# Kernel tuning notes

Hardware: AMD Instinct MI355X
Metric: run time of the kernel (lower is better)

Reference implementation:

```python
import jax, jax.numpy as jnp
import numpy as np

HIDDEN = 768
INTER = 3072
HEADS = 12
HEAD_DIM = INTER // HEADS  # 256
LN_EPS = 1e-6
R_SOFTPLUS_0 = 1.442695041


def setup_inputs() -> dict:
    key = jax.random.key(0)
    ks = jax.random.split(key, 12)
    s = 0.02
    inp = {
        "hidden_states": jax.random.normal(ks[0], (8, 4096, HIDDEN), dtype=jnp.float32),
        "pooling_query": jax.random.normal(ks[1], (1, 1, HIDDEN), dtype=jnp.float32) * s,
        "Wq": jax.random.normal(ks[2], (HIDDEN, INTER), dtype=jnp.float32) * s,
        "bq": jnp.zeros((INTER,), dtype=jnp.float32),
        "Wk": jax.random.normal(ks[3], (HIDDEN, INTER), dtype=jnp.float32) * s,
        "bk": jnp.zeros((INTER,), dtype=jnp.float32),
        "Wv": jax.random.normal(ks[4], (HIDDEN, INTER), dtype=jnp.float32) * s,
        "bv": jnp.zeros((INTER,), dtype=jnp.float32),
        "Wp": jax.random.normal(ks[5], (INTER, HIDDEN), dtype=jnp.float32) * s,
        "bp": jnp.zeros((HIDDEN,), dtype=jnp.float32),
        "per_dim_scale": jnp.zeros((HEAD_DIM,), dtype=jnp.float32),
        "ln_w": jnp.ones((HIDDEN,), dtype=jnp.float32),
        "ln_b": jnp.zeros((HIDDEN,), dtype=jnp.float32),
    }
    return inp


def reference(hidden_states, pooling_query, Wq, bq, Wk, bk, Wv, bv, Wp, bp,
              per_dim_scale, ln_w, ln_b):
    B, S, _ = hidden_states.shape
    dt = hidden_states.dtype

    # Query: single pooling token, identical across batch -> [H, D]
    q = (pooling_query.reshape(1, HIDDEN) @ Wq + bq).reshape(HEADS, HEAD_DIM)
    # PerDimScale: q * (r_softplus0/sqrt(D)) * softplus(per_dim_scale)
    scale = (R_SOFTPLUS_0 / np.sqrt(HEAD_DIM)).astype(np.float32)
    q = q * (scale * jax.nn.softplus(per_dim_scale))

    # K/V projections: [B, S, H, D]
    k = (hidden_states @ Wk + bk).reshape(B, S, HEADS, HEAD_DIM)
    v = (hidden_states @ Wv + bv).reshape(B, S, HEADS, HEAD_DIM)

    # Single-query attention: logits [B, H, S]; scaling=1.0 (scale_logits_by_head_dims=False)
    # logit cap skipped (no_attention_logit_cap=True)
    logits = jnp.einsum("hd,bshd->bhs", q, k)
    attn = jax.nn.softmax(logits.astype(jnp.float32), axis=-1).astype(dt)

    # Weighted sum over seq: [B, H, D] -> concat heads -> [B, H*D]
    ctx = jnp.einsum("bhs,bshd->bhd", attn, v).reshape(B, HEADS * HEAD_DIM)

    out = ctx @ Wp + bp  # [B, HIDDEN]
    # LayerNorm; note the original forward adds ones to ln weight in-place each call,
    # so effective weight for one call is (ln_w + 1).
    mean = jnp.mean(out, axis=-1, keepdims=True)
    var = jnp.var(out, axis=-1, keepdims=True)
    out = (out - mean) * jax.lax.rsqrt(var + LN_EPS) * (ln_w + 1.0) + ln_b

    pooled = out[:, None, :]  # [B, 1, HIDDEN]
    attn_weights = attn[:, :, None, :]  # [B, H, 1, S]
    return pooled, attn_weights
```

## Files before the change

### kernel.cpp

```cpp
#include <hip/hip_runtime.h>
#include <cstdint>
#include <cmath>

#define LN_EPS 1e-6f

#define N_QCH 24u
#define O_QPART 0u
#define O_Q     73728u
#define O_WK    76800u
#define O_PLOG  86016u
#define O_PHP   1658880u
#define N_SC    32
#define O_CTXP  4091904u
#define N_CCH   12
#define O_OUTP  4411392u
#define N_ICH   48

__device__ __forceinline__ float waveReduceSum(float v) {
#pragma unroll
    for (int o = 32; o >= 1; o >>= 1) v += __shfl_xor(v, o, 64);
    return v;
}
__device__ __forceinline__ float waveReduceMax(float v) {
#pragma unroll
    for (int o = 32; o >= 1; o >>= 1) v = fmaxf(v, __shfl_xor(v, o, 64));
    return v;
}

__global__ __launch_bounds__(256) void k1_qpart(const float* __restrict__ pq,
                                                const float* __restrict__ Wq,
                                                float* __restrict__ ws) {
    int h = blockIdx.x % 12;
    int ch = blockIdx.x / 12;
    int tid = threadIdx.x;
    int col = h * 256 + tid;
    int c0 = ch * 32;
    float acc = 0.f;
#pragma unroll 8
    for (int i = 0; i < 32; ++i) {
        int c = c0 + i;
        acc += pq[c] * Wq[c * 3072 + col];
    }
    ws[O_QPART + ch * 3072 + col] = acc;
}

__global__ __launch_bounds__(256) void k1b_qreduce(const float* __restrict__ bq,
                                                   const float* __restrict__ pds,
                                                   float* __restrict__ ws) {
    int j = blockIdx.x * 256 + threadIdx.x;
    float acc = bq[j];
#pragma unroll
    for (unsigned ch = 0; ch < N_QCH; ++ch) acc += ws[O_QPART + ch * 3072 + j];
    float x = pds[j & 255];
    float sp = (x > 20.f) ? x : log1pf(expf(x));
    const float scale = 1.442695041f / 16.0f;
    ws[O_Q + j] = acc * scale * sp;
}

__global__ __launch_bounds__(256) void k2_wkeff(const float* __restrict__ Wk,
                                                float* __restrict__ ws) {
    int c = blockIdx.x;
    int tid = threadIdx.x;
    int w = tid >> 6, lane = tid & 63;
    const float4* wk = reinterpret_cast<const float4*>(Wk + (size_t)c * 3072);
    const float4* qv = reinterpret_cast<const float4*>(ws + O_Q);
#pragma unroll
    for (int i = 0; i < 3; ++i) {
        int h = w * 3 + i;
        float4 a = wk[h * 64 + lane];
        float4 b = qv[h * 64 + lane];
        float d = a.x * b.x + a.y * b.y + a.z * b.z + a.w * b.w;
        d = waveReduceSum(d);
        if (lane == 0) ws[O_WK + c * 12 + h] = d;
    }
}

__global__ __launch_bounds__(256) void k3_logits(const float* __restrict__ hidden,
                                                 float* __restrict__ ws) {
    __shared__ float4 tile4[1536];
    __shared__ float4 wkb4[576];
    int blk = blockIdx.x;
    int q = blk & 3;
    int st = (blk >> 2) & 63;
    int b = blk >> 8;
    int s0 = st * 64;
    const float* hb = hidden + (size_t)(b * 4096 + s0) * 768;
    const float4* wkg4 = reinterpret_cast<const float4*>(ws + O_WK);
    int tid = threadIdx.x;
    int w = tid >> 6, lane = tid & 63;
    int rr[6], jj6[6];
#pragma unroll
    for (int it = 0; it < 6; ++it) {
        int idx = it * 256 + tid;
        rr[it] = idx / 24;
        jj6[it] = idx % 24;
    }
    for (int i = tid; i < 576; i += 256) wkb4[i] = wkg4[q * 576 + i];
    float4 v[6];
#pragma unroll
    for (int it = 0; it < 6; ++it)
        v[it] = reinterpret_cast<const float4*>(hb + rr[it] * 768 + q * 192)[jj6[it]];

    float acc[12];
#pragma unroll
    for (int h = 0; h < 12; ++h) acc[h] = 0.f;

#pragma unroll
    for (int cph = 0; cph < 2; ++cph) {
#pragma unroll
        for (int it = 0; it < 6; ++it)
            tile4[rr[it] * 24 + (jj6[it] ^ (rr[it] & 7))] = v[it];
        if (cph == 0) {
#pragma unroll
            for (int it = 0; it < 6; ++it)
                v[it] = reinterpret_cast<const float4*>(hb + rr[it] * 768 + q * 192 + 96)[jj6[it]];
        }
        __syncthreads();
#pragma unroll
        for (int jj = 0; jj < 6; ++jj) {
            int jcol = w * 6 + jj;
            float4 x = tile4[lane * 24 + (jcol ^ (lane & 7))];
            const float4* wr = &wkb4[cph * 288 + jcol * 12];
            float xc[4] = {x.x, x.y, x.z, x.w};
#pragma unroll
            for (int cc = 0; cc < 4; ++cc) {
                float4 w0 = wr[cc * 3 + 0], w1 = wr[cc * 3 + 1], w2 = wr[cc * 3 + 2];
                acc[0] += xc[cc] * w0.x;  acc[1] += xc[cc] * w0.y;  acc[2]  += xc[cc] * w0.z;  acc[3]  += xc[cc] * w0.w;
                acc[4] += xc[cc] * w1.x;  acc[5] += xc[cc] * w1.y;  acc[6]  += xc[cc] * w1.z;  acc[7]  += xc[cc] * w1.w;
                acc[8] += xc[cc] * w2.x;  acc[9] += xc[cc] * w2.y;  acc[10] += xc[cc] * w2.z;  acc[11] += xc[cc] * w2.w;
            }
        }
        __syncthreads();
    }
    float* red = reinterpret_cast<float*>(tile4);
#pragma unroll
    for (int h = 0; h < 12; ++h) red[(w * 12 + h) * 64 + lane] = acc[h];
    __syncthreads();
    float* plog = ws + O_PLOG;
    for (int idx = tid; idx < 768; idx += 256) {
        int h = idx / 64, r2 = idx & 63;
        float v2 = red[(0 + h) * 64 + r2] + red[(12 + h) * 64 + r2] +
                   red[(24 + h) * 64 + r2] + red[(36 + h) * 64 + r2];
        plog[(size_t)q * 393216 + (size_t)(b * 12 + h) * 4096 + s0 + r2] = v2;
    }
}

__global__ __launch_bounds__(256) void k4_softmax(const float* __restrict__ ws,
                                                  float* __restrict__ attn) {
    __shared__ float sh[4];
    int row = blockIdx.x;
    const float4* p0 = reinterpret_cast<const float4*>(ws + O_PLOG + (size_t)row * 4096);
    const float4* p1 = p0 + 98304;
    const float4* p2 = p0 + 196608;
    const float4* p3 = p0 + 294912;
    float* base = attn + (size_t)row * 4096;
    int tid = threadIdx.x;
    float4 x[4];
#pragma unroll
    for (int t = 0; t < 4; ++t) {
        float4 a = p0[t * 256 + tid], c = p1[t * 256 + tid];
        float4 d = p2[t * 256 + tid], e = p3[t * 256 + tid];
        x[t].x = (a.x + c.x) + (d.x + e.x);
        x[t].y = (a.y + c.y) + (d.y + e.y);
        x[t].z = (a.z + c.z) + (d.z + e.z);
        x[t].w = (a.w + c.w) + (d.w + e.w);
    }
    float m = -1e30f;
#pragma unroll
    for (int t = 0; t < 4; ++t)
        m = fmaxf(m, fmaxf(fmaxf(x[t].x, x[t].y), fmaxf(x[t].z, x[t].w)));
    m = waveReduceMax(m);
    if ((tid & 63) == 0) sh[tid >> 6] = m;
    __syncthreads();
    m = fmaxf(fmaxf(sh[0], sh[1]), fmaxf(sh[2], sh[3]));
    __syncthreads();
    float s = 0.f;
#pragma unroll
    for (int t = 0; t < 4; ++t) {
        x[t].x = expf(x[t].x - m); x[t].y = expf(x[t].y - m);
        x[t].z = expf(x[t].z - m); x[t].w = expf(x[t].w - m);
        s += x[t].x + x[t].y + x[t].z + x[t].w;
    }
    s = waveReduceSum(s);
    if ((tid & 63) == 0) sh[tid >> 6] = s;
    __syncthreads();
    s = sh[0] + sh[1] + sh[2] + sh[3];
    float inv = 1.0f / s;
#pragma unroll
    for (int t = 0; t < 4; ++t) {
        x[t].x *= inv; x[t].y *= inv; x[t].z *= inv; x[t].w *= inv;
        reinterpret_cast<float4*>(base)[t * 256 + tid] = x[t];
    }
}

__global__ __launch_bounds__(256) void k5_phpart(const float* __restrict__ hidden,
                                                 const float* __restrict__ attn,
                                                 float* __restrict__ ws) {
    __shared__ float4 sh4[12 * 4 * 64];
    int blk = blockIdx.x;
    int sc = blk & 31;
    int ct = (blk >> 5) % 3;
    int b = blk / 96;
    int tid = threadIdx.x;
    int w = tid >> 6, lane = tid & 63;
    int c = ct * 256 + lane * 4;
    int s0 = sc * 128;
    const float* hb = hidden + (size_t)(b * 4096 + s0) * 768 + c;
    const float* ab = attn + (size_t)b * 49152 + s0 + w;
    float4 acc[12];
#pragma unroll
    for (int h = 0; h < 12; ++h) acc[h] = make_float4(0.f, 0.f, 0.f, 0.f);
    for (int g = 0; g < 32; ++g) {
        float4 x = *reinterpret_cast<const float4*>(hb + (size_t)(g * 4 + w) * 768);
        float a[12];
#pragma unroll
        for (int h = 0; h < 12; ++h) a[h] = ab[h * 4096 + g * 4];
#pragma unroll
        for (int h = 0; h < 12; ++h) {
            acc[h].x += a[h] * x.x; acc[h].y += a[h] * x.y;
            acc[h].z += a[h] * x.z; acc[h].w += a[h] * x.w;
        }
    }
#pragma unroll
    for (int h = 0; h < 12; ++h) sh4[(h * 4 + w) * 64 + lane] = acc[h];
    __syncthreads();
    float* php = ws + O_PHP;
#pragma unroll
    for (int i = 0; i < 3; ++i) {
        int h = w * 3 + i;
        float4 a = sh4[(h * 4 + 0) * 64 + lane];
        float4 b2 = sh4[(h * 4 + 1) * 64 + lane];
        float4 c2 = sh4[(h * 4 + 2) * 64 + lane];
        float4 d = sh4[(h * 4 + 3) * 64 + lane];
        float4 r;
        r.x = (a.x + b2.x) + (c2.x + d.x);
        r.y = (a.y + b2.y) + (c2.y + d.y);
        r.z = (a.z + b2.z) + (c2.z + d.z);
        r.w = (a.w + b2.w) + (c2.w + d.w);
        *reinterpret_cast<float4*>(php + (size_t)(sc * 96 + b * 12 + h) * 768 + c) = r;
    }
}

__global__ __launch_bounds__(256) void k7_ctxpart(const float* __restrict__ Wv,
                                                  float* __restrict__ ws) {
    __shared__ float phl[512];
    int blk = blockIdx.x;
    int jt = blk % 12, cch = blk / 12;
    int tid = threadIdx.x;
    const float* php = ws + O_PHP;
#pragma unroll
    for (int t = 0; t < 2; ++t) {
        int idx = t * 256 + tid;
        int b = idx >> 6, cc = idx & 63;
        int c = cch * 64 + cc;
        const float* p = php + (size_t)(b * 12 + jt) * 768 + c;
        float s = 0.f;
#pragma unroll
        for (int sc = 0; sc < N_SC; ++sc) s += p[(size_t)sc * 73728];
        phl[idx] = s;
    }
    __syncthreads();
    int j = jt * 256 + tid;
    float acc[8];
#pragma unroll
    for (int b = 0; b < 8; ++b) acc[b] = 0.f;
    for (int cc = 0; cc < 64; ++cc) {
        int c = cch * 64 + cc;
        float wv = Wv[(size_t)c * 3072 + j];
#pragma unroll
        for (int b = 0; b < 8; ++b) acc[b] += phl[b * 64 + cc] * wv;
    }
#pragma unroll
    for (int b = 0; b < 8; ++b)
        ws[O_CTXP + (size_t)(cch * 8 + b) * 3072 + j] = acc[b];
}

__global__ __launch_bounds__(256) void k8_outpart(const float* __restrict__ Wp,
                                                  const float* __restrict__ bv,
                                                  float* __restrict__ ws) {
    __shared__ float ctxl[512];
    int blk = blockIdx.x;
    int jt = blk % 3, ich = blk / 3;
    int tid = threadIdx.x;
#pragma unroll
    for (int t = 0; t < 2; ++t) {
        int idx = t * 256 + tid;
        int b = idx >> 6, ii = idx & 63;
        int i = ich * 64 + ii;
        float s = bv[i];
#pragma unroll
        for (int cch = 0; cch < N_CCH; ++cch)
            s += ws[O_CTXP + (size_t)(cch * 8 + b) * 3072 + i];
        ctxl[idx] = s;
    }
    __syncthreads();
    int j = jt * 256 + tid;
    float acc[8];
#pragma unroll
    for (int b = 0; b < 8; ++b) acc[b] = 0.f;
    for (int ii = 0; ii < 64; ++ii) {
        int i = ich * 64 + ii;
        float wp = Wp[(size_t)i * 768 + j];
#pragma unroll
        for (int b = 0; b < 8; ++b) acc[b] += ctxl[b * 64 + ii] * wp;
    }
#pragma unroll
    for (int b = 0; b < 8; ++b)
        ws[O_OUTP + (size_t)(ich * 8 + b) * 768 + j] = acc[b];
}

__global__ __launch_bounds__(256) void k9_ln(const float* __restrict__ bp,
                                             const float* __restrict__ ln_w,
                                             const float* __restrict__ ln_b,
                                             const float* __restrict__ ws,
                                             float* __restrict__ pooled) {
    __shared__ float sh[8];
    int b = blockIdx.x, tid = threadIdx.x;
    const float* op = ws + O_OUTP;
    float vals[3];
    float lsum = 0.f, lsq = 0.f;
#pragma unroll
    for (int t = 0; t < 3; ++t) {
        int j = t * 256 + tid;
        float v = bp[j];
#pragma unroll
        for (int ich = 0; ich < N_ICH; ++ich) v += op[(size_t)(ich * 8 + b) * 768 + j];
        vals[t] = v; lsum += v; lsq += v * v;
    }
    lsum = waveReduceSum(lsum);
    lsq = waveReduceSum(lsq);
    if ((tid & 63) == 0) { sh[tid >> 6] = lsum; sh[4 + (tid >> 6)] = lsq; }
    __syncthreads();
    float mean = (sh[0] + sh[1] + sh[2] + sh[3]) * (1.f / 768.f);
    float var = (sh[4] + sh[5] + sh[6] + sh[7]) * (1.f / 768.f) - mean * mean;
    float inv = rsqrtf(var + LN_EPS);
#pragma unroll
    for (int t = 0; t < 3; ++t) {
        int j = t * 256 + tid;
        pooled[b * 768 + j] = (vals[t] - mean) * inv * (ln_w[j] + 1.f) + ln_b[j];
    }
}

extern "C" void kernel_launch(void* const* d_in, const int* in_sizes, int n_in,
                              void* d_out, int out_size, void* d_ws, size_t ws_size,
                              hipStream_t stream) {
    const float* hidden = (const float*)d_in[0];
    const float* pq     = (const float*)d_in[1];
    const float* Wq     = (const float*)d_in[2];
    const float* bq     = (const float*)d_in[3];
    const float* Wk     = (const float*)d_in[4];
    const float* Wv     = (const float*)d_in[6];
    const float* bv     = (const float*)d_in[7];
    const float* Wp     = (const float*)d_in[8];
    const float* bp     = (const float*)d_in[9];
    const float* pds    = (const float*)d_in[10];
    const float* ln_w   = (const float*)d_in[11];
    const float* ln_b   = (const float*)d_in[12];
    float* out = (float*)d_out;
    float* ws  = (float*)d_ws;
    float* pooled = out;
    float* attn   = out + 6144;

    k1_qpart   <<<288, 256, 0, stream>>>(pq, Wq, ws);
    k1b_qreduce<<<12, 256, 0, stream>>>(bq, pds, ws);
    k2_wkeff   <<<768, 256, 0, stream>>>(Wk, ws);
    k3_logits  <<<2048, 256, 0, stream>>>(hidden, ws);
    k4_softmax <<<96, 256, 0, stream>>>(ws, attn);
    k5_phpart  <<<768, 256, 0, stream>>>(hidden, attn, ws);
    k7_ctxpart <<<144, 256, 0, stream>>>(Wv, ws);
    k8_outpart <<<144, 256, 0, stream>>>(Wp, bv, ws);
    k9_ln      <<<8, 256, 0, stream>>>(bp, ln_w, ln_b, ws, pooled);
}
```

Before: 271.8 us.

## Double-buffer k3_logits LDS tile in four smaller chunks, drop trailing barrier

The logits kernel now stages each 64-row slice of hidden states in four 48-column chunks instead of two 96-column chunks. It ping-pongs between two shared-memory buffers, so the barrier at the end of each chunk iteration can be removed. Each thread holds three prefetched float4 registers instead of six, which lowers register pressure and may allow higher occupancy. The cost is more loop iterations with less work per barrier and a narrower XOR swizzle that could raise LDS bank conflicts.

After: 266.7 us (median of 2 runs). Within noise of the previous version (-1.9%).

```diff
diff --git a/kernel.cpp b/kernel.cpp
--- a/kernel.cpp
+++ b/kernel.cpp
@@ -77,50 +77,50 @@
 
 __global__ __launch_bounds__(256) void k3_logits(const float* __restrict__ hidden,
                                                  float* __restrict__ ws) {
-    __shared__ float4 tile4[1536];
+    __shared__ float4 tile4[2][768];
     __shared__ float4 wkb4[576];
     int blk = blockIdx.x;
     int q = blk & 3;
     int st = (blk >> 2) & 63;
     int b = blk >> 8;
     int s0 = st * 64;
-    const float* hb = hidden + (size_t)(b * 4096 + s0) * 768;
+    const float* hb = hidden + (size_t)(b * 4096 + s0) * 768 + q * 192;
     const float4* wkg4 = reinterpret_cast<const float4*>(ws + O_WK);
     int tid = threadIdx.x;
     int w = tid >> 6, lane = tid & 63;
-    int rr[6], jj6[6];
-#pragma unroll
-    for (int it = 0; it < 6; ++it) {
-        int idx = it * 256 + tid;
-        rr[it] = idx / 24;
-        jj6[it] = idx % 24;
-    }
     for (int i = tid; i < 576; i += 256) wkb4[i] = wkg4[q * 576 + i];
-    float4 v[6];
-#pragma unroll
-    for (int it = 0; it < 6; ++it)
-        v[it] = reinterpret_cast<const float4*>(hb + rr[it] * 768 + q * 192)[jj6[it]];
+    int rr[3], jj[3];
+#pragma unroll
+    for (int t = 0; t < 3; ++t) {
+        int idx = t * 256 + tid;
+        rr[t] = idx / 12;
+        jj[t] = idx % 12;
+    }
+    float4 v[3];
+#pragma unroll
+    for (int t = 0; t < 3; ++t)
+        v[t] = *reinterpret_cast<const float4*>(hb + rr[t] * 768 + jj[t] * 4);
 
     float acc[12];
 #pragma unroll
     for (int h = 0; h < 12; ++h) acc[h] = 0.f;
 
-#pragma unroll
-    for (int cph = 0; cph < 2; ++cph) {
-#pragma unroll
-        for (int it = 0; it < 6; ++it)
-            tile4[rr[it] * 24 + (jj6[it] ^ (rr[it] & 7))] = v[it];
-        if (cph == 0) {
-#pragma unroll
-            for (int it = 0; it < 6; ++it)
-                v[it] = reinterpret_cast<const float4*>(hb + rr[it] * 768 + q * 192 + 96)[jj6[it]];
+    for (int ck = 0; ck < 4; ++ck) {
+        float4* buf = tile4[ck & 1];
+#pragma unroll
+        for (int t = 0; t < 3; ++t)
+            buf[rr[t] * 12 + (jj[t] ^ (rr[t] & 3))] = v[t];
+        if (ck < 3) {
+#pragma unroll
+            for (int t = 0; t < 3; ++t)
+                v[t] = *reinterpret_cast<const float4*>(hb + rr[t] * 768 + (ck + 1) * 48 + jj[t] * 4);
         }
         __syncthreads();
 #pragma unroll
-        for (int jj = 0; jj < 6; ++jj) {
-            int jcol = w * 6 + jj;
-            float4 x = tile4[lane * 24 + (jcol ^ (lane & 7))];
-            const float4* wr = &wkb4[cph * 288 + jcol * 12];
+        for (int j2 = 0; j2 < 3; ++j2) {
+            int jcol = w * 3 + j2;
+            float4 x = buf[lane * 12 + (jcol ^ (lane & 3))];
+            const float4* wr = &wkb4[(ck * 48 + jcol * 4) * 3];
             float xc[4] = {x.x, x.y, x.z, x.w};
 #pragma unroll
             for (int cc = 0; cc < 4; ++cc) {
@@ -130,7 +130,6 @@
                 acc[8] += xc[cc] * w2.x;  acc[9] += xc[cc] * w2.y;  acc[10] += xc[cc] * w2.z;  acc[11] += xc[cc] * w2.w;
             }
         }
-        __syncthreads();
     }
     float* red = reinterpret_cast<float*>(tile4);
 #pragma unroll
@@ -139,9 +138,9 @@
     float* plog = ws + O_PLOG;
     for (int idx = tid; idx < 768; idx += 256) {
         int h = idx / 64, r2 = idx & 63;
-        float v2 = red[(0 + h) * 64 + r2] + red[(12 + h) * 64 + r2] +
+        float vv = red[(0 + h) * 64 + r2] + red[(12 + h) * 64 + r2] +
                    red[(24 + h) * 64 + r2] + red[(36 + h) * 64 + r2];
-        plog[(size_t)q * 393216 + (size_t)(b * 12 + h) * 4096 + s0 + r2] = v2;
+        plog[(size_t)q * 393216 + (size_t)(b * 12 + h) * 4096 + s0 + r2] = vv;
     }
 }
 
```
